# Performance work log

Hardware: AMD Instinct MI355X
Metric: run time of the kernel (lower is better)

Reference implementation:

```python
import jax
import jax.numpy as jnp
import numpy as np
from jax import lax

B = 256
H = W = 64
N_ACTIONS = 18
N_EXPERTS = 8
HIDDEN = 1024
LATENT = 256
EXPERT_DIM = 512
TOP_K = 2
CONV_OUT = 64 * H * W  # padding=1, k=3 convs preserve HxW


def setup_inputs() -> dict:
    key = jax.random.key(0)
    ks = jax.random.split(key, 18)

    def rn(k, shape, fan_in):
        # kaiming-ish scale, keeps activations sane
        return jax.random.normal(k, shape, jnp.float32) * np.float32(np.sqrt(2.0 / fan_in))

    return {
        "pixel_obs": jax.random.normal(ks[0], (B, 1, H, W), jnp.float32),
        # conv weights in torch OIHW layout
        "conv1_w": rn(ks[1], (16, 1, 3, 3), 9),
        "conv1_b": jnp.zeros((16,), jnp.float32),
        "conv2_w": rn(ks[2], (32, 16, 3, 3), 16 * 9),
        "conv2_b": jnp.zeros((32,), jnp.float32),
        "conv3_w": rn(ks[3], (64, 32, 3, 3), 32 * 9),
        "conv3_b": jnp.zeros((64,), jnp.float32),
        # linear weights stored [in, out]
        "fc1_w": rn(ks[4], (CONV_OUT, HIDDEN), CONV_OUT),
        "fc1_b": jnp.zeros((HIDDEN,), jnp.float32),
        "fc2_w": rn(ks[5], (HIDDEN, LATENT), HIDDEN),
        "fc2_b": jnp.zeros((LATENT,), jnp.float32),
        "gate_w": rn(ks[6], (LATENT, N_EXPERTS), LATENT),
        "gate_b": jnp.zeros((N_EXPERTS,), jnp.float32),
        # all experts stacked: [E, in, out]
        "exp_w1": rn(ks[7], (N_EXPERTS, LATENT, EXPERT_DIM), LATENT),
        "exp_b1": jnp.zeros((N_EXPERTS, EXPERT_DIM), jnp.float32),
        "exp_w2": rn(ks[8], (N_EXPERTS, EXPERT_DIM, N_ACTIONS), EXPERT_DIM),
        "exp_b2": jnp.zeros((N_EXPERTS, N_ACTIONS), jnp.float32),
    }


def _conv(x, w, b):
    y = lax.conv_general_dilated(
        x, w, window_strides=(1, 1), padding="SAME",
        dimension_numbers=("NCHW", "OIHW", "NCHW"))
    return jax.nn.relu(y + b[None, :, None, None])


def reference(pixel_obs, conv1_w, conv1_b, conv2_w, conv2_b, conv3_w, conv3_b,
              fc1_w, fc1_b, fc2_w, fc2_b, gate_w, gate_b,
              exp_w1, exp_b1, exp_w2, exp_b2):
    h = _conv(pixel_obs, conv1_w, conv1_b)
    h = _conv(h, conv2_w, conv2_b)
    h = _conv(h, conv3_w, conv3_b)          # [B, 64, H, W]
    flat = h.reshape(h.shape[0], -1)         # NCHW flatten matches torch .view
    s = jax.nn.relu(flat @ fc1_w + fc1_b)
    s = jax.nn.relu(s @ fc2_w + fc2_b)       # shared features [B, LATENT]

    gate_probs = jax.nn.softmax(s @ gate_w + gate_b, axis=1)  # [B, E]
    top_v, top_i = lax.top_k(gate_probs, TOP_K)               # [B, K]
    top_v = top_v / jnp.sum(top_v, axis=1, keepdims=True)

    # dense per-expert compute, as in the original (all experts on all tokens)
    eh = jax.nn.relu(jnp.einsum("bl,elh->beh", s, exp_w1) + exp_b1[None])
    eo = jnp.einsum("beh,eha->bea", eh, exp_w2) + exp_b2[None]  # [B, E, A]

    # fused gather + weighted combine (replaces the python double loop)
    sel = jnp.take_along_axis(eo, top_i[:, :, None], axis=1)    # [B, K, A]
    action_logits = jnp.sum(top_v[:, :, None] * sel, axis=1)    # [B, A]
    return action_logits, gate_probs
```

## Files before the change

### kernel.cpp

```cpp
#include <hip/hip_runtime.h>

typedef _Float16 f16x8 __attribute__((ext_vector_type(8)));
typedef float f32x4 __attribute__((ext_vector_type(4)));

__global__ void prepack_w(const float* __restrict__ w, _Float16* __restrict__ ph,
                          _Float16* __restrict__ pl, int COUT, int CIN, int KPAD)
{
  const int idx = blockIdx.x * 256 + threadIdx.x;
  const int KTOT = 3 * KPAD;
  if (idx >= COUT * KTOT) return;
  const int oc = idx / KTOT;
  const int rem = idx - oc * KTOT;
  const int y = rem / KPAD;
  const int kk = rem - y * KPAD;
  float v = 0.f;
  if (kk < 3 * CIN) {
    const int tx = kk / CIN;
    const int ic = kk - tx * CIN;
    v = w[((size_t)oc * CIN + ic) * 9 + y * 3 + tx];
  }
  const _Float16 h = (_Float16)v;
  ph[idx] = h;
  pl[idx] = (_Float16)((v - (float)h) * 2048.0f);
}

__global__ __launch_bounds__(256)
void conv1_k(const float* __restrict__ obs, const float* __restrict__ w,
             const float* __restrict__ bias, _Float16* __restrict__ outh,
             _Float16* __restrict__ outl)
{
  const int rg = blockIdx.x;
  const int b = blockIdx.y;
  const int tid = threadIdx.x;
  const int lr = tid >> 6;
  const int col = tid & 63;
  __shared__ float xs[6][66];
  __shared__ float wb[9][16];
  for (int idx = tid; idx < 6 * 66; idx += 256) {
    const int r = idx / 66, c = idx - (idx / 66) * 66;
    const int gr = rg * 4 - 1 + r, gc = c - 1;
    xs[r][c] = (gr >= 0 && gr < 64 && gc >= 0 && gc < 64)
                   ? obs[(size_t)b * 4096 + gr * 64 + gc] : 0.f;
  }
  if (tid < 144) wb[tid / 16][tid & 15] = w[(tid & 15) * 9 + tid / 16];
  __syncthreads();
  float acc[16];
#pragma unroll
  for (int o = 0; o < 16; ++o) acc[o] = bias[o];
#pragma unroll
  for (int ty = 0; ty < 3; ++ty)
#pragma unroll
    for (int tx = 0; tx < 3; ++tx) {
      const float x = xs[lr + ty][col + tx];
#pragma unroll
      for (int o = 0; o < 16; ++o) acc[o] = fmaf(x, wb[ty * 3 + tx][o], acc[o]);
    }
  const size_t base = ((size_t)(b * 64 + rg * 4 + lr) * 64 + col) * 16;
#pragma unroll
  for (int o = 0; o < 16; ++o) {
    const float v = fmaxf(acc[o], 0.f);
    const _Float16 h = (_Float16)v;
    outh[base + o] = h;
    outl[base + o] = (_Float16)((v - (float)h) * 2048.0f);
  }
}

template<int CIN, int COUT>
__global__ __launch_bounds__(256)
void conv_mfma(const _Float16* __restrict__ inh, const _Float16* __restrict__ inl,
               const _Float16* __restrict__ wph, const _Float16* __restrict__ wpl,
               const float* __restrict__ bias,
               _Float16* __restrict__ outh, _Float16* __restrict__ outl)
{
  constexpr int KFX = (3 * CIN + 31) / 32;
  constexpr int KPAD = KFX * 32;
  constexpr int KTOT = 3 * KPAD;
  constexpr int CP = CIN + 8;
  constexpr int NF = COUT / 32;
  const int rp = blockIdx.x;
  const int b  = blockIdx.y;
  const int r0 = rp * 2;
  const int tid = threadIdx.x;
  const int lane = tid & 63;
  const int wid = tid >> 6;
  const int wm = wid >> 1;
  const int wn = wid & 1;

  __shared__ _Float16 xh[4][68][CP];
  __shared__ _Float16 xl[4][68][CP];

  constexpr int CH = CIN / 8;
  for (int idx = tid; idx < 4 * 68 * CH; idx += 256) {
    const int r = idx / (68 * CH);
    const int rem = idx - r * 68 * CH;
    const int hc = rem / CH;
    const int ch = rem - hc * CH;
    const int gr = r0 - 1 + r;
    const int gc = hc - 1;
    uint4 vh = {0, 0, 0, 0}, vl = {0, 0, 0, 0};
    if (gr >= 0 && gr < 64 && gc >= 0 && gc < 64) {
      const size_t base = ((size_t)(b * 64 + gr) * 64 + gc) * CIN + ch * 8;
      vh = *(const uint4*)(inh + base);
      vl = *(const uint4*)(inl + base);
    }
    *(uint4*)&xh[r][hc][ch * 8] = vh;
    *(uint4*)&xl[r][hc][ch * 8] = vl;
  }
  __syncthreads();

  f32x4 accm[4][NF];
  f32x4 accc[4][NF];
#pragma unroll
  for (int mf = 0; mf < 4; ++mf)
#pragma unroll
    for (int nf = 0; nf < NF; ++nf) { accm[mf][nf] = {}; accc[mf][nf] = {}; }

  const int lm = lane & 15;
  const int ch8 = (lane >> 4) * 8;

#pragma unroll
  for (int kf = 0; kf < 3 * KFX; ++kf) {
    const int y = kf / KFX;
    const int fx = kf - y * KFX;
    const int kk = fx * 32 + ch8;
    f16x8 bh[NF], bl[NF];
#pragma unroll
    for (int nf = 0; nf < NF; ++nf) {
      const int oc = wn * (16 * NF) + nf * 16 + lm;
      bh[nf] = *(const f16x8*)(wph + (size_t)oc * KTOT + kf * 32 + ch8);
      bl[nf] = *(const f16x8*)(wpl + (size_t)oc * KTOT + kf * 32 + ch8);
    }
#pragma unroll
    for (int mf = 0; mf < 4; ++mf) {
      const int col = mf * 16 + lm;
      const f16x8 ah = *(const f16x8*)&xh[wm + y][col + kk / CIN][kk % CIN];
      const f16x8 al = *(const f16x8*)&xl[wm + y][col + kk / CIN][kk % CIN];
#pragma unroll
      for (int nf = 0; nf < NF; ++nf) {
        accm[mf][nf] = __builtin_amdgcn_mfma_f32_16x16x32_f16(ah, bh[nf], accm[mf][nf], 0, 0, 0);
        accc[mf][nf] = __builtin_amdgcn_mfma_f32_16x16x32_f16(ah, bl[nf], accc[mf][nf], 0, 0, 0);
        accc[mf][nf] = __builtin_amdgcn_mfma_f32_16x16x32_f16(al, bh[nf], accc[mf][nf], 0, 0, 0);
      }
    }
  }

  const int orow = r0 + wm;
#pragma unroll
  for (int nf = 0; nf < NF; ++nf) {
    const int oc = wn * (16 * NF) + nf * 16 + lm;
    const float bv = bias[oc];
#pragma unroll
    for (int mf = 0; mf < 4; ++mf) {
#pragma unroll
      for (int r = 0; r < 4; ++r) {
        const int x = mf * 16 + (lane >> 4) * 4 + r;
        const float v = fmaxf(accm[mf][nf][r] + accc[mf][nf][r] * (1.0f / 2048.0f) + bv, 0.f);
        const _Float16 h = (_Float16)v;
        const size_t oi = ((size_t)(b * 64 + orow) * 64 + x) * COUT + oc;
        outh[oi] = h;
        outl[oi] = (_Float16)((v - (float)h) * 2048.0f);
      }
    }
  }
}

__global__ __launch_bounds__(512, 2)
void fc1_gemm_v3(const _Float16* __restrict__ Ahi, const _Float16* __restrict__ Alo,
                 const float* __restrict__ W, float* __restrict__ P)
{
  const int sk = blockIdx.x;
  const int nt = blockIdx.y;
  const int nc0 = nt * 128;
  const int tid = threadIdx.x;
  const int lane = tid & 63;
  const int wid = tid >> 6;
  const int wm = wid >> 1;
  const int wn = wid & 1;

  __shared__ _Float16 Ah[2][256][32];
  __shared__ _Float16 Al[2][256][32];
  __shared__ _Float16 Bh[2][128][32];
  __shared__ _Float16 Bl[2][128][32];

  f32x4 accm[4][4] = {};
  f32x4 accc[4][4] = {};

  const int nl = tid & 127;
  const int kq = tid >> 7;
  const int bslot = kq ^ ((nl >> 1) & 3);

  const size_t kbase = (size_t)sk * 8192;
  constexpr int NIT = 256;

  const int Rbase = wid * 32;
  const int lrow0 = Rbase + (lane >> 2);
  const int lrow1 = Rbase + 16 + (lane >> 2);
  const int sd = lane & 3;
  const int ssrc0 = sd ^ ((lrow0 >> 1) & 3);
  const int ssrc1 = sd ^ ((lrow1 >> 1) & 3);
  const size_t goff0 = (size_t)lrow0 * 262144 + ssrc0 * 8;
  const size_t goff1 = (size_t)lrow1 * 262144 + ssrc1 * 8;

#define ISSUE_A(p, k0)                                                                     \
  {                                                                                        \
    __builtin_amdgcn_global_load_lds(                                                      \
        (const __attribute__((address_space(1))) unsigned int*)(Ahi + goff0 + (k0)),       \
        (__attribute__((address_space(3))) unsigned int*)&Ah[p][Rbase][0], 16, 0, 0);      \
    __builtin_amdgcn_global_load_lds(                                                      \
        (const __attribute__((address_space(1))) unsigned int*)(Ahi + goff1 + (k0)),       \
        (__attribute__((address_space(3))) unsigned int*)&Ah[p][Rbase + 16][0], 16, 0, 0); \
    __builtin_amdgcn_global_load_lds(                                                      \
        (const __attribute__((address_space(1))) unsigned int*)(Alo + goff0 + (k0)),       \
        (__attribute__((address_space(3))) unsigned int*)&Al[p][Rbase][0], 16, 0, 0);      \
    __builtin_amdgcn_global_load_lds(                                                      \
        (const __attribute__((address_space(1))) unsigned int*)(Alo + goff1 + (k0)),       \
        (__attribute__((address_space(3))) unsigned int*)&Al[p][Rbase + 16][0], 16, 0, 0); \
  }

#define LOAD_W(k0, wr)                                                     \
  {                                                                        \
    const size_t jb = (k0) + kq * 8;                                       \
    _Pragma("unroll") for (int i = 0; i < 8; ++i) {                        \
      const size_t j = jb + i;                                             \
      const size_t wrow = ((j & 63) << 12) + (j >> 6);                     \
      wr[i] = W[wrow * 1024 + nc0 + nl];                                   \
    }                                                                      \
  }

#define WRITE_B(p, wr)                                                     \
  {                                                                        \
    f16x8 hv, lv;                                                          \
    _Pragma("unroll") for (int i = 0; i < 8; ++i) {                        \
      const _Float16 h = (_Float16)wr[i];                                  \
      hv[i] = h;                                                           \
      lv[i] = (_Float16)((wr[i] - (float)h) * 2048.0f);                    \
    }                                                                      \
    *(f16x8*)&Bh[p][nl][bslot * 8] = hv;                                   \
    *(f16x8*)&Bl[p][nl][bslot * 8] = lv;                                   \
  }

  {
    float wr[8];
    ISSUE_A(0, kbase);
    LOAD_W(kbase, wr);
    WRITE_B(0, wr);
  }
  __syncthreads();

  const int q = lane >> 4;
  int p = 0;
  for (int it = 0; it < NIT; ++it) {
    float wr[8];
    const bool pf = (it + 1 < NIT);
    if (pf) {
      const size_t k0n = kbase + (size_t)(it + 1) * 32;
      ISSUE_A(p ^ 1, k0n);
      LOAD_W(k0n, wr);
    }

    f16x8 ah[4], al[4], bh[4], bl[4];
#pragma unroll
    for (int mf = 0; mf < 4; ++mf) {
      const int r = wm * 64 + mf * 16 + (lane & 15);
      const int s = (q ^ ((r >> 1) & 3)) * 8;
      ah[mf] = *(const f16x8*)&Ah[p][r][s];
      al[mf] = *(const f16x8*)&Al[p][r][s];
    }
#pragma unroll
    for (int nf = 0; nf < 4; ++nf) {
      const int n = wn * 64 + nf * 16 + (lane & 15);
      const int s = (q ^ ((n >> 1) & 3)) * 8;
      bh[nf] = *(const f16x8*)&Bh[p][n][s];
      bl[nf] = *(const f16x8*)&Bl[p][n][s];
    }
#pragma unroll
    for (int mf = 0; mf < 4; ++mf)
#pragma unroll
      for (int nf = 0; nf < 4; ++nf) {
        accm[mf][nf] = __builtin_amdgcn_mfma_f32_16x16x32_f16(ah[mf], bh[nf], accm[mf][nf], 0, 0, 0);
        accc[mf][nf] = __builtin_amdgcn_mfma_f32_16x16x32_f16(ah[mf], bl[nf], accc[mf][nf], 0, 0, 0);
        accc[mf][nf] = __builtin_amdgcn_mfma_f32_16x16x32_f16(al[mf], bh[nf], accc[mf][nf], 0, 0, 0);
      }

    if (pf) WRITE_B(p ^ 1, wr);
    __syncthreads();
    p ^= 1;
  }
#undef ISSUE_A
#undef LOAD_W
#undef WRITE_B

#pragma unroll
  for (int mf = 0; mf < 4; ++mf) {
    const int rbase = wm * 64 + mf * 16 + ((lane >> 4) << 2);
#pragma unroll
    for (int nf = 0; nf < 4; ++nf) {
      const int c = nc0 + wn * 64 + nf * 16 + (lane & 15);
#pragma unroll
      for (int r = 0; r < 4; ++r)
        P[((size_t)sk * 256 + rbase + r) * 1024 + c] =
            accm[mf][nf][r] + accc[mf][nf][r] * (1.0f / 2048.0f);
    }
  }
}

__global__ __launch_bounds__(256)
void fc1_reduce(const float* __restrict__ P, const float* __restrict__ bias,
                float* __restrict__ s1)
{
  const int idx = blockIdx.x * 256 + threadIdx.x;
  const int n = idx & 1023;
  float a = bias[n];
#pragma unroll 8
  for (int sk = 0; sk < 32; ++sk) a += P[(size_t)sk * 262144 + idx];
  s1[idx] = fmaxf(a, 0.f);
}

__global__ __launch_bounds__(256)
void fc2_k(const float* __restrict__ s1, const float* __restrict__ w,
           const float* __restrict__ b, float* __restrict__ s2)
{
  const int bb = blockIdx.x;
  const int t = threadIdx.x;
  __shared__ float xr[1024];
  for (int i = t; i < 1024; i += 256) xr[i] = s1[bb * 1024 + i];
  __syncthreads();
  float a0 = b[t], a1 = 0.f, a2 = 0.f, a3 = 0.f;
#pragma unroll 4
  for (int k = 0; k < 1024; k += 4) {
    a0 += xr[k + 0] * w[(k + 0) * 256 + t];
    a1 += xr[k + 1] * w[(k + 1) * 256 + t];
    a2 += xr[k + 2] * w[(k + 2) * 256 + t];
    a3 += xr[k + 3] * w[(k + 3) * 256 + t];
  }
  s2[bb * 256 + t] = fmaxf(a0 + a1 + a2 + a3, 0.f);
}

__global__ __launch_bounds__(64)
void gate_k(const float* __restrict__ s2, const float* __restrict__ gw,
            const float* __restrict__ gb, float* __restrict__ gate_out,
            int* __restrict__ topi, float* __restrict__ topv)
{
  const int bb = blockIdx.x;
  const int l = threadIdx.x;
  float part[8] = {};
  for (int k = l; k < 256; k += 64) {
    const float x = s2[bb * 256 + k];
#pragma unroll
    for (int e = 0; e < 8; ++e) part[e] += x * gw[k * 8 + e];
  }
#pragma unroll
  for (int off = 32; off > 0; off >>= 1)
#pragma unroll
    for (int e = 0; e < 8; ++e) part[e] += __shfl_down(part[e], off);

  if (l == 0) {
    float lg[8];
    float m = -1e30f;
#pragma unroll
    for (int e = 0; e < 8; ++e) { lg[e] = part[e] + gb[e]; m = fmaxf(m, lg[e]); }
    float s = 0.f;
    float p[8];
#pragma unroll
    for (int e = 0; e < 8; ++e) { p[e] = expf(lg[e] - m); s += p[e]; }
#pragma unroll
    for (int e = 0; e < 8; ++e) { p[e] = p[e] / s; gate_out[bb * 8 + e] = p[e]; }
    int i0 = 0;
#pragma unroll
    for (int e = 1; e < 8; ++e) if (p[e] > p[i0]) i0 = e;
    int i1 = (i0 == 0) ? 1 : 0;
#pragma unroll
    for (int e = 0; e < 8; ++e) if (e != i0 && p[e] > p[i1]) i1 = e;
    const float v0 = p[i0], v1 = p[i1];
    topi[bb * 2 + 0] = i0; topi[bb * 2 + 1] = i1;
    topv[bb * 2 + 0] = v0 / (v0 + v1); topv[bb * 2 + 1] = v1 / (v0 + v1);
  }
}

__global__ __launch_bounds__(256)
void expert_k(const float* __restrict__ s2, const float* __restrict__ w1,
              const float* __restrict__ b1, const float* __restrict__ w2,
              const float* __restrict__ b2, const int* __restrict__ topi,
              const float* __restrict__ topv, float* __restrict__ out)
{
  const int bb = blockIdx.x;
  const int t = threadIdx.x;
  __shared__ float xr[256];
  __shared__ float eh[512];
  __shared__ float partial[18][8];
  xr[t] = s2[bb * 256 + t];
  float logit = 0.f;
  for (int kk = 0; kk < 2; ++kk) {
    __syncthreads();
    const int e = topi[bb * 2 + kk];
    const float tv = topv[bb * 2 + kk];
    const float* W1 = w1 + (size_t)e * 256 * 512;
    float a0 = b1[e * 512 + t], a1 = b1[e * 512 + 256 + t];
#pragma unroll 4
    for (int k = 0; k < 256; ++k) {
      const float x = xr[k];
      a0 = fmaf(x, W1[k * 512 + t], a0);
      a1 = fmaf(x, W1[k * 512 + 256 + t], a1);
    }
    eh[t] = fmaxf(a0, 0.f);
    eh[256 + t] = fmaxf(a1, 0.f);
    __syncthreads();
    if (t < 144) {
      const int a = t >> 3, q2 = t & 7;
      const float* W2 = w2 + (size_t)e * 512 * 18;
      float pp = 0.f;
      for (int h = q2 * 64; h < q2 * 64 + 64; ++h) pp = fmaf(eh[h], W2[h * 18 + a], pp);
      partial[a][q2] = pp;
    }
    __syncthreads();
    if (t < 18) {
      float s = b2[e * 18 + t];
#pragma unroll
      for (int q2 = 0; q2 < 8; ++q2) s += partial[t][q2];
      logit = fmaf(tv, s, logit);
    }
  }
  if (t < 18) out[bb * 18 + t] = logit;
}

extern "C" void kernel_launch(void* const* d_in, const int* in_sizes, int n_in,
                              void* d_out, int out_size, void* d_ws, size_t ws_size,
                              hipStream_t stream) {
  const float* obs     = (const float*)d_in[0];
  const float* conv1_w = (const float*)d_in[1];
  const float* conv1_b = (const float*)d_in[2];
  const float* conv2_w = (const float*)d_in[3];
  const float* conv2_b = (const float*)d_in[4];
  const float* conv3_w = (const float*)d_in[5];
  const float* conv3_b = (const float*)d_in[6];
  const float* fc1_w   = (const float*)d_in[7];
  const float* fc1_b   = (const float*)d_in[8];
  const float* fc2_w   = (const float*)d_in[9];
  const float* fc2_b   = (const float*)d_in[10];
  const float* gate_w  = (const float*)d_in[11];
  const float* gate_b  = (const float*)d_in[12];
  const float* exp_w1  = (const float*)d_in[13];
  const float* exp_b1  = (const float*)d_in[14];
  const float* exp_w2  = (const float*)d_in[15];
  const float* exp_b2  = (const float*)d_in[16];

  char* ws = (char*)d_ws;
  const size_t MB = 1ull << 20;
  const size_t KB = 1ull << 10;
  _Float16* act1h = (_Float16*)(ws);
  _Float16* act1l = (_Float16*)(ws + 32 * MB);
  _Float16* act2h = (_Float16*)(ws + 64 * MB);
  _Float16* act2l = (_Float16*)(ws + 128 * MB);
  _Float16* act3h = (_Float16*)(ws + 192 * MB);
  _Float16* act3l = (_Float16*)(ws + 320 * MB);
  float*    P     = (float*)(ws);
  _Float16* wp2h  = (_Float16*)(ws + 448 * MB);
  _Float16* wp2l  = (_Float16*)(ws + 448 * MB + 64 * KB);
  _Float16* wp3h  = (_Float16*)(ws + 448 * MB + 128 * KB);
  _Float16* wp3l  = (_Float16*)(ws + 448 * MB + 192 * KB);
  float*    s2    = (float*)(ws + 448 * MB + 256 * KB);
  int*      topi  = (int*)(ws + 448 * MB + 512 * KB);
  float*    topv  = (float*)(ws + 448 * MB + 516 * KB);
  float*    s1    = (float*)(ws + 449 * MB);
  float*    out   = (float*)d_out;

  prepack_w<<<(32 * 192 + 255) / 256, 256, 0, stream>>>(conv2_w, wp2h, wp2l, 32, 16, 64);
  prepack_w<<<(64 * 288 + 255) / 256, 256, 0, stream>>>(conv3_w, wp3h, wp3l, 64, 32, 96);

  conv1_k<<<dim3(16, 256), 256, 0, stream>>>(obs, conv1_w, conv1_b, act1h, act1l);
  conv_mfma<16, 32><<<dim3(32, 256), 256, 0, stream>>>(act1h, act1l, wp2h, wp2l, conv2_b, act2h, act2l);
  conv_mfma<32, 64><<<dim3(32, 256), 256, 0, stream>>>(act2h, act2l, wp3h, wp3l, conv3_b, act3h, act3l);

  fc1_gemm_v3<<<dim3(32, 8), 512, 0, stream>>>(act3h, act3l, fc1_w, P);
  fc1_reduce<<<1024, 256, 0, stream>>>(P, fc1_b, s1);
  fc2_k<<<256, 256, 0, stream>>>(s1, fc2_w, fc2_b, s2);
  gate_k<<<256, 64, 0, stream>>>(s2, gate_w, gate_b, out + 256 * 18, topi, topv);
  expert_k<<<256, 256, 0, stream>>>(s2, exp_w1, exp_b1, exp_w2, exp_b2, topi, topv, out);
}
```

Before: 1.034 ms.

## Write conv3 output in NCHW via LDS staging so fc1 reads weights contiguously

conv3 now stages its output tile in shared memory and writes it to global memory in NCHW order with 16-byte vector stores. This lets the fc1 GEMM index its weight rows linearly instead of using the permuted row mapping needed for NHWC activations. The aim is more coalesced activation stores and more sequential weight reads in the large fc1 GEMM. The cost is extra LDS use and a block-wide barrier in conv3.

```diff
diff --git a/kernel.cpp b/kernel.cpp
--- a/kernel.cpp
+++ b/kernel.cpp
@@ -1,6 +1,7 @@
 #include <hip/hip_runtime.h>
 
 typedef _Float16 f16x8 __attribute__((ext_vector_type(8)));
+typedef _Float16 f16x4 __attribute__((ext_vector_type(4)));
 typedef float f32x4 __attribute__((ext_vector_type(4)));
 
 __global__ void prepack_w(const float* __restrict__ w, _Float16* __restrict__ ph,
@@ -65,7 +66,7 @@
   }
 }
 
-template<int CIN, int COUT>
+template<int CIN, int COUT, bool NCHW_OUT>
 __global__ __launch_bounds__(256)
 void conv_mfma(const _Float16* __restrict__ inh, const _Float16* __restrict__ inl,
                const _Float16* __restrict__ wph, const _Float16* __restrict__ wpl,
@@ -77,6 +78,8 @@
   constexpr int KTOT = 3 * KPAD;
   constexpr int CP = CIN + 8;
   constexpr int NF = COUT / 32;
+  constexpr int STO = NCHW_OUT ? COUT : 1;
+  constexpr int STP = NCHW_OUT ? 136 : 8;
   const int rp = blockIdx.x;
   const int b  = blockIdx.y;
   const int r0 = rp * 2;
@@ -88,6 +91,8 @@
 
   __shared__ _Float16 xh[4][68][CP];
   __shared__ _Float16 xl[4][68][CP];
+  __shared__ _Float16 st_h[STO][STP];
+  __shared__ _Float16 st_l[STO][STP];
 
   constexpr int CH = CIN / 8;
   for (int idx = tid; idx < 4 * 68 * CH; idx += 256) {
@@ -144,21 +149,52 @@
     }
   }
 
-  const int orow = r0 + wm;
-#pragma unroll
-  for (int nf = 0; nf < NF; ++nf) {
-    const int oc = wn * (16 * NF) + nf * 16 + lm;
-    const float bv = bias[oc];
-#pragma unroll
-    for (int mf = 0; mf < 4; ++mf) {
-#pragma unroll
-      for (int r = 0; r < 4; ++r) {
-        const int x = mf * 16 + (lane >> 4) * 4 + r;
-        const float v = fmaxf(accm[mf][nf][r] + accc[mf][nf][r] * (1.0f / 2048.0f) + bv, 0.f);
-        const _Float16 h = (_Float16)v;
-        const size_t oi = ((size_t)(b * 64 + orow) * 64 + x) * COUT + oc;
-        outh[oi] = h;
-        outl[oi] = (_Float16)((v - (float)h) * 2048.0f);
+  if constexpr (NCHW_OUT) {
+#pragma unroll
+    for (int nf = 0; nf < NF; ++nf) {
+      const int oc = wn * (16 * NF) + nf * 16 + lm;
+      const float bv = bias[oc];
+#pragma unroll
+      for (int mf = 0; mf < 4; ++mf) {
+        f16x4 hv, lv;
+#pragma unroll
+        for (int r = 0; r < 4; ++r) {
+          const float v = fmaxf(accm[mf][nf][r] + accc[mf][nf][r] * (1.0f / 2048.0f) + bv, 0.f);
+          const _Float16 h = (_Float16)v;
+          hv[r] = h;
+          lv[r] = (_Float16)((v - (float)h) * 2048.0f);
+        }
+        const int px = wm * 64 + mf * 16 + (lane >> 4) * 4;
+        *(f16x4*)&st_h[oc][px] = hv;
+        *(f16x4*)&st_l[oc][px] = lv;
+      }
+    }
+    __syncthreads();
+    const int oc2 = tid >> 2;
+    const int seg = tid & 3;
+    const size_t gb = ((size_t)b * COUT + oc2) * 4096 + r0 * 64 + seg * 32;
+#pragma unroll
+    for (int j2 = 0; j2 < 4; ++j2) {
+      *(uint4*)(outh + gb + j2 * 8) = *(const uint4*)&st_h[oc2][seg * 32 + j2 * 8];
+      *(uint4*)(outl + gb + j2 * 8) = *(const uint4*)&st_l[oc2][seg * 32 + j2 * 8];
+    }
+  } else {
+    const int orow = r0 + wm;
+#pragma unroll
+    for (int nf = 0; nf < NF; ++nf) {
+      const int oc = wn * (16 * NF) + nf * 16 + lm;
+      const float bv = bias[oc];
+#pragma unroll
+      for (int mf = 0; mf < 4; ++mf) {
+#pragma unroll
+        for (int r = 0; r < 4; ++r) {
+          const int x = mf * 16 + (lane >> 4) * 4 + r;
+          const float v = fmaxf(accm[mf][nf][r] + accc[mf][nf][r] * (1.0f / 2048.0f) + bv, 0.f);
+          const _Float16 h = (_Float16)v;
+          const size_t oi = ((size_t)(b * 64 + orow) * 64 + x) * COUT + oc;
+          outh[oi] = h;
+          outl[oi] = (_Float16)((v - (float)h) * 2048.0f);
+        }
       }
     }
   }
@@ -221,9 +257,7 @@
   {                                                                        \
     const size_t jb = (k0) + kq * 8;                                       \
     _Pragma("unroll") for (int i = 0; i < 8; ++i) {                        \
-      const size_t j = jb + i;                                             \
-      const size_t wrow = ((j & 63) << 12) + (j >> 6);                     \
-      wr[i] = W[wrow * 1024 + nc0 + nl];                                   \
+      wr[i] = W[(jb + i) * 1024 + nc0 + nl];                               \
     }                                                                      \
   }
 
@@ -468,8 +502,8 @@
   prepack_w<<<(64 * 288 + 255) / 256, 256, 0, stream>>>(conv3_w, wp3h, wp3l, 64, 32, 96);
 
   conv1_k<<<dim3(16, 256), 256, 0, stream>>>(obs, conv1_w, conv1_b, act1h, act1l);
-  conv_mfma<16, 32><<<dim3(32, 256), 256, 0, stream>>>(act1h, act1l, wp2h, wp2l, conv2_b, act2h, act2l);
-  conv_mfma<32, 64><<<dim3(32, 256), 256, 0, stream>>>(act2h, act2l, wp3h, wp3l, conv3_b, act3h, act3l);
+  conv_mfma<16, 32, false><<<dim3(32, 256), 256, 0, stream>>>(act1h, act1l, wp2h, wp2l, conv2_b, act2h, act2l);
+  conv_mfma<32, 64, true ><<<dim3(32, 256), 256, 0, stream>>>(act2h, act2l, wp3h, wp3l, conv3_b, act3h, act3l);
 
   fc1_gemm_v3<<<dim3(32, 8), 512, 0, stream>>>(act3h, act3l, fc1_w, P);
   fc1_reduce<<<1024, 256, 0, stream>>>(P, fc1_b, s1);
```

Result: no change. 1.051 ms (+1.6%).
